# Kernel optimization log

Hardware: AMD Instinct MI355X
Metric: run time of the kernel (lower is better)

## Reference

```python
import jax, jax.numpy as jnp
import numpy as np

N, D, P = 8000, 256, 128


def setup_inputs() -> dict:
    key = jax.random.key(0)
    k_adj, k_emb, k_att, k_w, k_f, k_idx = jax.random.split(key, 6)
    # symmetric binary adjacency, avg degree ~ 32, self-loops guarantee deg > 0
    a = (jax.random.uniform(k_adj, (N, N)) < 0.004).astype(jnp.float32)
    adj = jnp.maximum(a, a.T)
    adj = jnp.maximum(adj, jnp.eye(N, dtype=jnp.float32))
    embeddings = jax.random.normal(k_emb, (N, D), dtype=jnp.float32)
    w_att = jax.random.normal(k_att, (D, D), dtype=jnp.float32) / np.sqrt(D)
    b_att = jnp.zeros((D,), dtype=jnp.float32)
    w_weight = jax.random.normal(k_w, (1, 2 * D), dtype=jnp.float32) / np.sqrt(2 * D)
    w_final = jax.random.normal(k_f, (1, 1), dtype=jnp.float32)
    pos_idx = jnp.sort(jax.random.randint(k_idx, (P,), 0, N))  # sorted like torch.nonzero
    return {"adj": adj, "embeddings": embeddings, "w_att": w_att, "b_att": b_att,
            "w_weight": w_weight, "w_final": w_final, "pos_idx": pos_idx}


def reference(adj, embeddings, w_att, b_att, w_weight, w_final, pos_idx):
    n = adj.shape[0]
    # normalized adjacencies (buffers in the torch module)
    dinv = jnp.power(jnp.sum(adj, axis=1), -0.5)          # deg^{-1/2}, [N]
    adj_rcnorm = dinv[None, :] * adj * dinv[:, None]      # d_i^-.5 A_ij d_j^-.5
    adj_rnorm = dinv[None, :] * adj                       # A_ij d_j^-.5
    # one-hot indicator vector (torch forward receives this as `inputs`)
    inputs = jnp.zeros((n,), dtype=adj.dtype).at[pos_idx].set(1.0)
    # gather positive embeddings and adjacency rows (torch.nonzero gather)
    pos_emb = embeddings[pos_idx]                         # [P, D]
    pos_adj = adj[pos_idx]                                # [P, N]
    proj = pos_emb @ w_att.T + b_att                      # [P, D]
    att_scores = pos_adj * (proj @ embeddings.T)          # [P, N], masked scores
    att_probs = jax.nn.softmax(att_scores, axis=0)        # softmax over positives
    context = att_probs.T @ pos_emb                       # [N, D]
    cat = jnp.concatenate([embeddings, context], axis=1)  # [N, 2D]
    mutual_w = jax.nn.sigmoid(cat @ w_weight.T)[:, 0]     # [N]
    # two-hop sparse propagation (expressed as dense matvecs, same math)
    out = adj_rcnorm.T @ inputs                           # [N]
    out = out * mutual_w                                  # elementwise reweight
    out = adj_rnorm.T @ out                               # [N]
    out = out * w_final[0, 0]                             # final Linear(1,1,no bias)
    return out[None, :]                                   # [1, N]
```

## Files before the change

### kernel.cpp

```cpp
#include <hip/hip_runtime.h>
#include <math.h>

#define N 8000
#define D 256
#define P 128

__global__ __launch_bounds__(256) void deg_kernel(const float* __restrict__ adj,
                                                  float* __restrict__ dinv) {
    int row = blockIdx.x;
    const float4* r = (const float4*)(adj + (size_t)row * N);
    float s = 0.f;
    for (int i = threadIdx.x; i < N / 4; i += 256) {
        float4 a = r[i];
        s += a.x + a.y + a.z + a.w;
    }
    for (int off = 32; off > 0; off >>= 1) s += __shfl_down(s, off, 64);
    __shared__ float red[4];
    int lane = threadIdx.x & 63, wave = threadIdx.x >> 6;
    if (lane == 0) red[wave] = s;
    __syncthreads();
    if (threadIdx.x == 0) {
        float t = red[0] + red[1] + red[2] + red[3];
        dinv[row] = rsqrtf(t);
    }
}

__global__ __launch_bounds__(256) void proj_kernel(const float* __restrict__ emb,
                                                   const float* __restrict__ w_att,
                                                   const float* __restrict__ b_att,
                                                   const float* __restrict__ w_weight,
                                                   const int* __restrict__ pos_idx,
                                                   float* __restrict__ projT,
                                                   float* __restrict__ pe2) {
    int p = blockIdx.x;
    int row = pos_idx[p];
    __shared__ float e[D];
    __shared__ float red[D];
    int tid = threadIdx.x;
    e[tid] = emb[(size_t)row * D + tid];
    __syncthreads();
    float acc = b_att[tid];
    const float* wrow = w_att + (size_t)tid * D;
    #pragma unroll 4
    for (int k = 0; k < D; k++) acc += e[k] * wrow[k];
    projT[(size_t)tid * P + p] = acc;
    red[tid] = e[tid] * w_weight[D + tid];
    __syncthreads();
    for (int s = 128; s > 0; s >>= 1) {
        if (tid < s) red[tid] += red[tid + s];
        __syncthreads();
    }
    if (tid == 0) pe2[p] = red[0];
}

__global__ __launch_bounds__(256) void attn_kernel(const float* __restrict__ emb,
                                                   const float* __restrict__ projT,
                                                   const float* __restrict__ adj,
                                                   const int* __restrict__ pos_idx,
                                                   const float* __restrict__ pe2,
                                                   const float* __restrict__ w_weight,
                                                   float* __restrict__ mutual_w) {
    __shared__ float At[32][68];
    __shared__ float B[32][128];
    __shared__ float S[64][129];
    __shared__ int   posrow[P];
    __shared__ float pe2s[P];
    __shared__ float w1[D];

    int tid = threadIdx.x;
    int tx = tid & 15;
    int ty = tid >> 4;
    int n0 = blockIdx.x * 64;

    if (tid < P) { posrow[tid] = pos_idx[tid]; pe2s[tid] = pe2[tid]; }
    w1[tid] = w_weight[tid];

    float acc[4][8];
    #pragma unroll
    for (int i = 0; i < 4; i++)
        #pragma unroll
        for (int j = 0; j < 8; j++) acc[i][j] = 0.f;

    for (int d0 = 0; d0 < D; d0 += 32) {
        __syncthreads();
        {
            int nn = tid >> 2;
            int dk0 = (tid & 3) * 8;
            const float* src = emb + (size_t)(n0 + nn) * D + d0 + dk0;
            float4 v0 = *(const float4*)(src);
            float4 v1 = *(const float4*)(src + 4);
            At[dk0 + 0][nn] = v0.x; At[dk0 + 1][nn] = v0.y;
            At[dk0 + 2][nn] = v0.z; At[dk0 + 3][nn] = v0.w;
            At[dk0 + 4][nn] = v1.x; At[dk0 + 5][nn] = v1.y;
            At[dk0 + 6][nn] = v1.z; At[dk0 + 7][nn] = v1.w;
        }
        #pragma unroll
        for (int r = 0; r < 4; r++) {
            int f = (r * 256 + tid) * 4;
            int dk = f >> 7, pp = f & 127;
            *(float4*)&B[dk][pp] = *(const float4*)(projT + (size_t)(d0 + dk) * P + pp);
        }
        __syncthreads();
        #pragma unroll
        for (int dk = 0; dk < 32; dk++) {
            float4 a4 = *(const float4*)&At[dk][tx * 4];
            float b[8];
            *(float4*)&b[0] = *(const float4*)&B[dk][ty * 8];
            *(float4*)&b[4] = *(const float4*)&B[dk][ty * 8 + 4];
            #pragma unroll
            for (int j = 0; j < 8; j++) {
                acc[0][j] += a4.x * b[j];
                acc[1][j] += a4.y * b[j];
                acc[2][j] += a4.z * b[j];
                acc[3][j] += a4.w * b[j];
            }
        }
    }
    #pragma unroll
    for (int j = 0; j < 8; j++) {
        int p = ty * 8 + j;
        float4 m4 = *(const float4*)(adj + (size_t)posrow[p] * N + n0 + tx * 4);
        S[tx * 4 + 0][p] = acc[0][j] * m4.x;
        S[tx * 4 + 1][p] = acc[1][j] * m4.y;
        S[tx * 4 + 2][p] = acc[2][j] * m4.z;
        S[tx * 4 + 3][p] = acc[3][j] * m4.w;
    }
    __syncthreads();
    if (tid < 64) {
        int n = n0 + tid;
        float mm = -1e30f;
        for (int p = 0; p < P; p++) mm = fmaxf(mm, S[tid][p]);
        float Z = 0.f, ape = 0.f;
        for (int p = 0; p < P; p++) {
            float ex = __expf(S[tid][p] - mm);
            Z += ex;
            ape += ex * pe2s[p];
        }
        float e1 = 0.f;
        const float4* er = (const float4*)(emb + (size_t)n * D);
        #pragma unroll 4
        for (int d = 0; d < D / 4; d++) {
            float4 ev = er[d];
            e1 += ev.x * w1[4 * d] + ev.y * w1[4 * d + 1] +
                  ev.z * w1[4 * d + 2] + ev.w * w1[4 * d + 3];
        }
        float logit = e1 + ape / Z;
        mutual_w[n] = 1.f / (1.f + __expf(-logit));
    }
}

__global__ __launch_bounds__(256) void out1_kernel(const float* __restrict__ adj,
                                                   const int* __restrict__ pos_idx,
                                                   const float* __restrict__ dinv,
                                                   const float* __restrict__ mutual_w,
                                                   float* __restrict__ v) {
    __shared__ int posrow[P];
    __shared__ float fac[P];
    int tid = threadIdx.x;
    if (tid < P) {
        int r = pos_idx[tid];
        posrow[tid] = r;
        float f = dinv[r];
        if (tid > 0 && pos_idx[tid - 1] == r) f = 0.f;
        fac[tid] = f;
    }
    __syncthreads();
    int n = blockIdx.x * 256 + tid;
    if (n < N) {
        float s = 0.f;
        #pragma unroll 4
        for (int p = 0; p < P; p++) s += adj[(size_t)posrow[p] * N + n] * fac[p];
        v[n] = s * dinv[n] * mutual_w[n];
    }
}

__global__ __launch_bounds__(256) void final_kernel(const float* __restrict__ adj,
                                                    const float* __restrict__ v,
                                                    const float* __restrict__ dinv,
                                                    const float* __restrict__ w_final,
                                                    float* __restrict__ out) {
    int row = blockIdx.x;
    const float4* r = (const float4*)(adj + (size_t)row * N);
    const float4* vv = (const float4*)v;
    float s = 0.f;
    for (int i = threadIdx.x; i < N / 4; i += 256) {
        float4 a = r[i];
        float4 b = vv[i];
        s += a.x * b.x + a.y * b.y + a.z * b.z + a.w * b.w;
    }
    for (int off = 32; off > 0; off >>= 1) s += __shfl_down(s, off, 64);
    __shared__ float red[4];
    int lane = threadIdx.x & 63, wave = threadIdx.x >> 6;
    if (lane == 0) red[wave] = s;
    __syncthreads();
    if (threadIdx.x == 0)
        out[row] = (red[0] + red[1] + red[2] + red[3]) * dinv[row] * w_final[0];
}

extern "C" void kernel_launch(void* const* d_in, const int* in_sizes, int n_in,
                              void* d_out, int out_size, void* d_ws, size_t ws_size,
                              hipStream_t stream) {
    const float* adj    = (const float*)d_in[0];
    const float* emb    = (const float*)d_in[1];
    const float* w_att  = (const float*)d_in[2];
    const float* b_att  = (const float*)d_in[3];
    const float* w_w    = (const float*)d_in[4];
    const float* w_f    = (const float*)d_in[5];
    const int*   pos    = (const int*)d_in[6];
    float* out = (float*)d_out;

    float* ws     = (float*)d_ws;
    float* dinv   = ws;
    float* projT  = dinv + N;
    float* pe2    = projT + (size_t)D * P;
    float* mutual = pe2 + P;
    float* v      = mutual + N;

    deg_kernel  <<<N,              256, 0, stream>>>(adj, dinv);
    proj_kernel <<<P,              256, 0, stream>>>(emb, w_att, b_att, w_w, pos, projT, pe2);
    attn_kernel <<<N / 64,         256, 0, stream>>>(emb, projT, adj, pos, pe2, w_w, mutual);
    out1_kernel <<<(N + 255) / 256, 256, 0, stream>>>(adj, pos, dinv, mutual, v);
    final_kernel<<<N,              256, 0, stream>>>(adj, v, dinv, w_f, out);
}
```

Before: 446.8 us.

## Compress adjacency to bitmask in degree pass and fuse out1 into attention

Result: faster. 407.2 us (-8.9%).

```diff
diff --git a/kernel.cpp b/kernel.cpp
--- a/kernel.cpp
+++ b/kernel.cpp
@@ -4,25 +4,34 @@
 #define N 8000
 #define D 256
 #define P 128
+#define NW 250
 
 __global__ __launch_bounds__(256) void deg_kernel(const float* __restrict__ adj,
-                                                  float* __restrict__ dinv) {
+                                                  float* __restrict__ dinv,
+                                                  unsigned int* __restrict__ msk) {
     int row = blockIdx.x;
+    int tid = threadIdx.x;
     const float4* r = (const float4*)(adj + (size_t)row * N);
     float s = 0.f;
-    for (int i = threadIdx.x; i < N / 4; i += 256) {
-        float4 a = r[i];
-        s += a.x + a.y + a.z + a.w;
+    if (tid < NW) {
+        unsigned int m = 0;
+        #pragma unroll
+        for (int j = 0; j < 8; j++) {
+            float4 a = r[tid * 8 + j];
+            s += a.x + a.y + a.z + a.w;
+            m |= (a.x != 0.f ? 1u : 0u) << (4 * j + 0);
+            m |= (a.y != 0.f ? 1u : 0u) << (4 * j + 1);
+            m |= (a.z != 0.f ? 1u : 0u) << (4 * j + 2);
+            m |= (a.w != 0.f ? 1u : 0u) << (4 * j + 3);
+        }
+        msk[(size_t)row * NW + tid] = m;
     }
     for (int off = 32; off > 0; off >>= 1) s += __shfl_down(s, off, 64);
     __shared__ float red[4];
-    int lane = threadIdx.x & 63, wave = threadIdx.x >> 6;
+    int lane = tid & 63, wave = tid >> 6;
     if (lane == 0) red[wave] = s;
     __syncthreads();
-    if (threadIdx.x == 0) {
-        float t = red[0] + red[1] + red[2] + red[3];
-        dinv[row] = rsqrtf(t);
-    }
+    if (tid == 0) dinv[row] = rsqrtf(red[0] + red[1] + red[2] + red[3]);
 }
 
 __global__ __launch_bounds__(256) void proj_kernel(const float* __restrict__ emb,
@@ -55,16 +64,19 @@
 
 __global__ __launch_bounds__(256) void attn_kernel(const float* __restrict__ emb,
                                                    const float* __restrict__ projT,
-                                                   const float* __restrict__ adj,
+                                                   const unsigned int* __restrict__ msk,
                                                    const int* __restrict__ pos_idx,
                                                    const float* __restrict__ pe2,
                                                    const float* __restrict__ w_weight,
-                                                   float* __restrict__ mutual_w) {
+                                                   const float* __restrict__ dinv,
+                                                   float* __restrict__ v) {
     __shared__ float At[32][68];
     __shared__ float B[32][128];
     __shared__ float S[64][129];
+    __shared__ float R[16][68];
     __shared__ int   posrow[P];
     __shared__ float pe2s[P];
+    __shared__ float fac[P];
     __shared__ float w1[D];
 
     int tid = threadIdx.x;
@@ -72,7 +84,14 @@
     int ty = tid >> 4;
     int n0 = blockIdx.x * 64;
 
-    if (tid < P) { posrow[tid] = pos_idx[tid]; pe2s[tid] = pe2[tid]; }
+    if (tid < P) {
+        int r0 = pos_idx[tid];
+        posrow[tid] = r0;
+        pe2s[tid] = pe2[tid];
+        float f = dinv[r0];
+        if (tid > 0 && pos_idx[tid - 1] == r0) f = 0.f;
+        fac[tid] = f;
+    }
     w1[tid] = w_weight[tid];
 
     float acc[4][8];
@@ -80,6 +99,7 @@
     for (int i = 0; i < 4; i++)
         #pragma unroll
         for (int j = 0; j < 8; j++) acc[i][j] = 0.f;
+    float e1 = 0.f;
 
     for (int d0 = 0; d0 < D; d0 += 32) {
         __syncthreads();
@@ -115,17 +135,37 @@
                 acc[3][j] += a4.w * b[j];
             }
         }
-    }
+        if (tid < 64) {
+            float t = 0.f;
+            #pragma unroll
+            for (int dk = 0; dk < 32; dk++) t += At[dk][tid] * w1[d0 + dk];
+            e1 += t;
+        }
+    }
+
+    float vp[4] = {0.f, 0.f, 0.f, 0.f};
+    int wbase = (n0 + tx * 4) >> 5;
+    int bsh = (tx & 7) * 4;
     #pragma unroll
     for (int j = 0; j < 8; j++) {
         int p = ty * 8 + j;
-        float4 m4 = *(const float4*)(adj + (size_t)posrow[p] * N + n0 + tx * 4);
-        S[tx * 4 + 0][p] = acc[0][j] * m4.x;
-        S[tx * 4 + 1][p] = acc[1][j] * m4.y;
-        S[tx * 4 + 2][p] = acc[2][j] * m4.z;
-        S[tx * 4 + 3][p] = acc[3][j] * m4.w;
-    }
-    __syncthreads();
+        unsigned int w = msk[(size_t)posrow[p] * NW + wbase];
+        float fp = fac[p];
+        float m0 = (w >> (bsh + 0)) & 1u ? 1.f : 0.f;
+        float m1 = (w >> (bsh + 1)) & 1u ? 1.f : 0.f;
+        float m2 = (w >> (bsh + 2)) & 1u ? 1.f : 0.f;
+        float m3 = (w >> (bsh + 3)) & 1u ? 1.f : 0.f;
+        S[tx * 4 + 0][p] = acc[0][j] * m0;
+        S[tx * 4 + 1][p] = acc[1][j] * m1;
+        S[tx * 4 + 2][p] = acc[2][j] * m2;
+        S[tx * 4 + 3][p] = acc[3][j] * m3;
+        vp[0] += m0 * fp; vp[1] += m1 * fp;
+        vp[2] += m2 * fp; vp[3] += m3 * fp;
+    }
+    #pragma unroll
+    for (int i = 0; i < 4; i++) R[ty][tx * 4 + i] = vp[i];
+    __syncthreads();
+
     if (tid < 64) {
         int n = n0 + tid;
         float mm = -1e30f;
@@ -136,65 +176,35 @@
             Z += ex;
             ape += ex * pe2s[p];
         }
-        float e1 = 0.f;
-        const float4* er = (const float4*)(emb + (size_t)n * D);
-        #pragma unroll 4
-        for (int d = 0; d < D / 4; d++) {
-            float4 ev = er[d];
-            e1 += ev.x * w1[4 * d] + ev.y * w1[4 * d + 1] +
-                  ev.z * w1[4 * d + 2] + ev.w * w1[4 * d + 3];
-        }
+        float vs = 0.f;
+        #pragma unroll
+        for (int t = 0; t < 16; t++) vs += R[t][tid];
         float logit = e1 + ape / Z;
-        mutual_w[n] = 1.f / (1.f + __expf(-logit));
-    }
-}
-
-__global__ __launch_bounds__(256) void out1_kernel(const float* __restrict__ adj,
-                                                   const int* __restrict__ pos_idx,
-                                                   const float* __restrict__ dinv,
-                                                   const float* __restrict__ mutual_w,
-                                                   float* __restrict__ v) {
-    __shared__ int posrow[P];
-    __shared__ float fac[P];
-    int tid = threadIdx.x;
-    if (tid < P) {
-        int r = pos_idx[tid];
-        posrow[tid] = r;
-        float f = dinv[r];
-        if (tid > 0 && pos_idx[tid - 1] == r) f = 0.f;
-        fac[tid] = f;
-    }
-    __syncthreads();
-    int n = blockIdx.x * 256 + tid;
-    if (n < N) {
-        float s = 0.f;
-        #pragma unroll 4
-        for (int p = 0; p < P; p++) s += adj[(size_t)posrow[p] * N + n] * fac[p];
-        v[n] = s * dinv[n] * mutual_w[n];
-    }
-}
-
-__global__ __launch_bounds__(256) void final_kernel(const float* __restrict__ adj,
-                                                    const float* __restrict__ v,
+        float mw = 1.f / (1.f + __expf(-logit));
+        v[n] = vs * dinv[n] * mw;
+    }
+}
+
+__global__ __launch_bounds__(256) void final_kernel(const unsigned int* __restrict__ msk,
+                                                    const float* __restrict__ vvec,
                                                     const float* __restrict__ dinv,
                                                     const float* __restrict__ w_final,
                                                     float* __restrict__ out) {
-    int row = blockIdx.x;
-    const float4* r = (const float4*)(adj + (size_t)row * N);
-    const float4* vv = (const float4*)v;
+    int wave = threadIdx.x >> 6, lane = threadIdx.x & 63;
+    int row = blockIdx.x * 4 + wave;
+    const unsigned int* mrow = msk + (size_t)row * NW;
     float s = 0.f;
-    for (int i = threadIdx.x; i < N / 4; i += 256) {
-        float4 a = r[i];
-        float4 b = vv[i];
-        s += a.x * b.x + a.y * b.y + a.z * b.z + a.w * b.w;
+    for (int wi = lane; wi < NW; wi += 64) {
+        unsigned int m = mrow[wi];
+        int base = wi * 32;
+        while (m) {
+            int k = __ffs(m) - 1;
+            s += vvec[base + k];
+            m &= m - 1;
+        }
     }
     for (int off = 32; off > 0; off >>= 1) s += __shfl_down(s, off, 64);
-    __shared__ float red[4];
-    int lane = threadIdx.x & 63, wave = threadIdx.x >> 6;
-    if (lane == 0) red[wave] = s;
-    __syncthreads();
-    if (threadIdx.x == 0)
-        out[row] = (red[0] + red[1] + red[2] + red[3]) * dinv[row] * w_final[0];
+    if (lane == 0) out[row] = s * dinv[row] * w_final[0];
 }
 
 extern "C" void kernel_launch(void* const* d_in, const int* in_sizes, int n_in,
@@ -213,12 +223,11 @@
     float* dinv   = ws;
     float* projT  = dinv + N;
     float* pe2    = projT + (size_t)D * P;
-    float* mutual = pe2 + P;
-    float* v      = mutual + N;
-
-    deg_kernel  <<<N,              256, 0, stream>>>(adj, dinv);
-    proj_kernel <<<P,              256, 0, stream>>>(emb, w_att, b_att, w_w, pos, projT, pe2);
-    attn_kernel <<<N / 64,         256, 0, stream>>>(emb, projT, adj, pos, pe2, w_w, mutual);
-    out1_kernel <<<(N + 255) / 256, 256, 0, stream>>>(adj, pos, dinv, mutual, v);
-    final_kernel<<<N,              256, 0, stream>>>(adj, v, dinv, w_f, out);
-}
+    float* v      = pe2 + P;
+    unsigned int* msk = (unsigned int*)(v + N);
+
+    deg_kernel  <<<N,      256, 0, stream>>>(adj, dinv, msk);
+    proj_kernel <<<P,      256, 0, stream>>>(emb, w_att, b_att, w_w, pos, projT, pe2);
+    attn_kernel <<<N / 64, 256, 0, stream>>>(emb, projT, msk, pos, pe2, w_w, dinv, v);
+    final_kernel<<<N / 4,  256, 0, stream>>>(msk, v, dinv, w_f, out);
+}
```
